# Performance work log

Hardware: AMD Instinct MI355X
Metric: run time of the kernel (lower is better)

The kernel has to match this reference:

```python
import jax, jax.numpy as jnp
import numpy as np

DIM = 1024
NUM_HEADS = 16
HEAD_DIM = DIM // NUM_HEADS
SCALE = HEAD_DIM ** (-0.5)


def setup_inputs() -> dict:
    key = jax.random.key(0)
    ks = jax.random.split(key, 10)
    b, nq, nkv = 1, 4096, 4096
    s = DIM ** -0.5
    return {
        "q": jax.random.normal(ks[0], (b, nq, DIM), jnp.float32),
        "kv": jax.random.normal(ks[1], (b, nkv, DIM), jnp.float32),
        "q_w": jax.random.normal(ks[2], (DIM, DIM), jnp.float32) * s,
        "q_b": jnp.zeros((DIM,), jnp.float32),
        "k_w": jax.random.normal(ks[3], (DIM, DIM), jnp.float32) * s,
        "k_b": jnp.zeros((DIM,), jnp.float32),
        "v_w": jax.random.normal(ks[4], (DIM, DIM), jnp.float32) * s,
        "v_b": jnp.zeros((DIM,), jnp.float32),
        "o_w": jax.random.normal(ks[5], (DIM, DIM), jnp.float32) * s,
        "o_b": jnp.zeros((DIM,), jnp.float32),
    }


def reference(q, kv, q_w, q_b, k_w, k_b, v_w, v_b, o_w, o_b):
    b, nq, _ = q.shape
    nkv = kv.shape[1]
    h, c = NUM_HEADS, HEAD_DIM
    # projections (torch Linear: x @ W^T + b); split into heads
    qh = (q @ q_w.T + q_b).reshape(b, nq, h, c).transpose(0, 2, 1, 3)   # b h nq c
    kh = (kv @ k_w.T + k_b).reshape(b, nkv, h, c).transpose(0, 2, 1, 3)  # b h nkv c
    vh = (kv @ v_w.T + v_b).reshape(b, nkv, h, c).transpose(0, 2, 1, 3)  # b h nkv c
    # full attention score matrix (non-fused, as in source)
    attn = jnp.einsum('bhqc,bhkc->bhqk', qh, kh) * SCALE
    attn = jax.nn.softmax(attn, axis=-1)
    out = jnp.einsum('bhqk,bhkc->bhqc', attn, vh)  # b h nq c
    out = out.transpose(0, 2, 1, 3).reshape(b, nq, h * c)
    out = out @ o_w.T + o_b
    return out
```

## Files before the change

### kernel.cpp

```cpp
#include <hip/hip_runtime.h>


typedef unsigned short ushort_t;
typedef unsigned short ushort4v __attribute__((ext_vector_type(4)));
typedef unsigned short ushort8 __attribute__((ext_vector_type(8)));
typedef __bf16 bf16x8 __attribute__((ext_vector_type(8)));
typedef float f32x4 __attribute__((ext_vector_type(4)));
typedef float f32x16 __attribute__((ext_vector_type(16)));

#define SEQ 4096
#define DIM 1024
#define NH 16
#define HD 64
#define QSCALE 0.18033688011112042f

#define LSTR 40
#define ABUF (128 * LSTR)
#define BBUF (64 * LSTR)

__device__ inline ushort_t fcvt(float f) {
    return __builtin_bit_cast(ushort_t, (__bf16)f);
}
__device__ inline bf16x8 frag_of(ushort8 t) {
    return __builtin_bit_cast(bf16x8, t);
}
__device__ inline bf16x8 lds_frag(const ushort_t* p) {
    return frag_of(*(const ushort8*)p);
}

__global__ __launch_bounds__(256) void cvt2(
    const float* __restrict__ s0, ushort_t* __restrict__ d0,
    const float* __restrict__ s1, ushort_t* __restrict__ d1, int n8)
{
    const float* s = blockIdx.y ? s1 : s0;
    ushort_t*    d = blockIdx.y ? d1 : d0;
    int i = blockIdx.x * 256 + threadIdx.x;
    if (i >= n8) return;
    const f32x4* sp = (const f32x4*)s + (size_t)i * 2;
    f32x4 a = sp[0], b = sp[1];
    ushort8 o;
    for (int k = 0; k < 4; ++k) { o[k] = fcvt(a[k]); o[k + 4] = fcvt(b[k]); }
    *((ushort8*)d + i) = o;
}

__global__ __launch_bounds__(256) void cvt4(
    const float* __restrict__ s0, ushort_t* __restrict__ d0,
    const float* __restrict__ s1, ushort_t* __restrict__ d1,
    const float* __restrict__ s2, ushort_t* __restrict__ d2,
    const float* __restrict__ s3, ushort_t* __restrict__ d3, int n8)
{
    const float* ss[4] = {s0, s1, s2, s3};
    ushort_t*    dd[4] = {d0, d1, d2, d3};
    const float* s = ss[blockIdx.y];
    ushort_t*    d = dd[blockIdx.y];
    int i = blockIdx.x * 256 + threadIdx.x;
    if (i >= n8) return;
    const f32x4* sp = (const f32x4*)s + (size_t)i * 2;
    f32x4 a = sp[0], b = sp[1];
    ushort8 o;
    for (int k = 0; k < 4; ++k) { o[k] = fcvt(a[k]); o[k + 4] = fcvt(b[k]); }
    *((ushort8*)d + i) = o;
}

__device__ __attribute__((always_inline)) inline void gemm_core(
    const ushort_t* __restrict__ A, const ushort_t* __restrict__ W,
    int m0, int n0, int tid, f32x4 (&acc)[4][2], ushort_t* sA, ushort_t* sB)
{
    const int lane = tid & 63;
    const int quad = lane >> 4;
    const int l15  = lane & 15;
    const int wm   = (tid >> 6) >> 1;
    const int wn   = (tid >> 6) & 1;

    const int ar0 = tid >> 2;
    const int ar1 = (tid + 256) >> 2;
    const int ac  = (tid & 3) << 3;
    const int br  = tid >> 2;
    const ushort_t* Ag0 = A + (size_t)(m0 + ar0) * DIM + ac;
    const ushort_t* Ag1 = A + (size_t)(m0 + ar1) * DIM + ac;
    const ushort_t* Wg  = W + (size_t)(n0 + br) * DIM + ac;
    const int la0 = ar0 * LSTR + ac, la1 = ar1 * LSTR + ac, lb = br * LSTR + ac;

    *(ushort8*)(sA + la0) = *(const ushort8*)(Ag0);
    *(ushort8*)(sA + la1) = *(const ushort8*)(Ag1);
    *(ushort8*)(sB + lb)  = *(const ushort8*)(Wg);
    __syncthreads();

    for (int it = 0; it < DIM / 32; ++it) {
        const int cur = it & 1;
        const int ktn = (it + 1) * 32;
        ushort_t* aC = sA + cur * ABUF;
        ushort_t* bC = sB + cur * BBUF;

        ushort8 ga0, ga1, gb0;
        if (ktn < DIM) {
            ga0 = *(const ushort8*)(Ag0 + ktn);
            ga1 = *(const ushort8*)(Ag1 + ktn);
            gb0 = *(const ushort8*)(Wg + ktn);
        }

        bf16x8 af[4], bf[2];
        for (int i = 0; i < 4; ++i)
            af[i] = lds_frag(aC + (wm * 64 + i * 16 + l15) * LSTR + quad * 8);
        for (int j = 0; j < 2; ++j)
            bf[j] = lds_frag(bC + (wn * 32 + j * 16 + l15) * LSTR + quad * 8);
        for (int i = 0; i < 4; ++i)
            for (int j = 0; j < 2; ++j)
                acc[i][j] = __builtin_amdgcn_mfma_f32_16x16x32_bf16(
                    af[i], bf[j], acc[i][j], 0, 0, 0);

        if (ktn < DIM) {
            ushort_t* aN = sA + (cur ^ 1) * ABUF;
            ushort_t* bN = sB + (cur ^ 1) * BBUF;
            *(ushort8*)(aN + la0) = ga0;
            *(ushort8*)(aN + la1) = ga1;
            *(ushort8*)(bN + lb)  = gb0;
        }
        __syncthreads();
    }
}

__global__ __launch_bounds__(256) void proj3(
    const ushort_t* __restrict__ Qb, const ushort_t* __restrict__ KVb,
    const ushort_t* __restrict__ qwb, const ushort_t* __restrict__ kwb,
    const ushort_t* __restrict__ vwb,
    const float* __restrict__ q_b, const float* __restrict__ k_b,
    const float* __restrict__ v_b,
    ushort_t* __restrict__ Qp, ushort_t* __restrict__ Kp,
    ushort_t* __restrict__ VpT)
{
    __shared__ __align__(16) ushort_t sA[2 * ABUF];
    __shared__ __align__(16) ushort_t sB[2 * BBUF];

    const int z = blockIdx.z;
    const ushort_t* A = z ? KVb : Qb;
    const ushort_t* W = (z == 0) ? qwb : (z == 1 ? kwb : vwb);
    const float* bias = (z == 0) ? q_b : (z == 1 ? k_b : v_b);
    const int tid = threadIdx.x;
    const int m0 = blockIdx.y * 128;
    const int n0 = blockIdx.x * 64;

    f32x4 acc[4][2] = {};
    gemm_core(A, W, m0, n0, tid, acc, sA, sB);

    const int lane = tid & 63, quad = lane >> 4, l15 = lane & 15;
    const int wm = (tid >> 6) >> 1, wn = (tid >> 6) & 1;
    const float scale = (z == 0) ? QSCALE : 1.0f;

    for (int j = 0; j < 2; ++j) {
        int col = n0 + wn * 32 + j * 16 + l15;
        float bj = bias[col];
        for (int i = 0; i < 4; ++i) {
            int row = m0 + wm * 64 + i * 16 + quad * 4;
            if (z == 2) {
                ushort4v o4;
                for (int r = 0; r < 4; ++r) o4[r] = fcvt(acc[i][j][r] + bj);
                *(ushort4v*)(VpT + (size_t)col * SEQ + row) = o4;
            } else {
                ushort_t* C = z ? Kp : Qp;
                for (int r = 0; r < 4; ++r)
                    C[(size_t)(row + r) * DIM + col] =
                        fcvt((acc[i][j][r] + bj) * scale);
            }
        }
    }
}

__global__ __launch_bounds__(256) void gemm_out(
    const ushort_t* __restrict__ A, const ushort_t* __restrict__ W,
    const float* __restrict__ bias, float* __restrict__ C)
{
    __shared__ __align__(16) ushort_t sA[2 * ABUF];
    __shared__ __align__(16) ushort_t sB[2 * BBUF];

    const int tid = threadIdx.x;
    const int m0 = blockIdx.y * 128;
    const int n0 = blockIdx.x * 64;

    f32x4 acc[4][2] = {};
    gemm_core(A, W, m0, n0, tid, acc, sA, sB);

    const int lane = tid & 63, quad = lane >> 4, l15 = lane & 15;
    const int wm = (tid >> 6) >> 1, wn = (tid >> 6) & 1;
    for (int j = 0; j < 2; ++j) {
        int col = n0 + wn * 32 + j * 16 + l15;
        float bj = bias[col];
        for (int i = 0; i < 4; ++i) {
            int row = m0 + wm * 64 + i * 16 + quad * 4;
            for (int r = 0; r < 4; ++r)
                C[(size_t)(row + r) * DIM + col] = acc[i][j][r] + bj;
        }
    }
}

#define BUFE (2 * 64 * 72)
__global__ __launch_bounds__(256) void attn_kernel(
    const ushort_t* __restrict__ Q, const ushort_t* __restrict__ K,
    const ushort_t* __restrict__ VT, ushort_t* __restrict__ O)
{
    __shared__ __align__(16) ushort_t sB[2 * BUFE];

    const int tid  = threadIdx.x;
    const int w    = tid >> 6;
    const int lane = tid & 63;
    const int l31  = lane & 31;
    const int hi   = lane >> 5;
    const int h    = blockIdx.x;
    const int q0   = blockIdx.y * 128 + w * 32;
    const int hHD  = h * HD;

    const int srow0 = tid >> 3;
    const int srow1 = (tid + 256) >> 3;
    const int sch   = (tid & 7) << 3;
    const ushort_t* Kg0 = K  + (size_t)srow0 * DIM + hHD + sch;
    const ushort_t* Kg1 = K  + (size_t)srow1 * DIM + hHD + sch;
    const ushort_t* Vg0 = VT + (size_t)(hHD + srow0) * SEQ + sch;
    const ushort_t* Vg1 = VT + (size_t)(hHD + srow1) * SEQ + sch;
    const int l0 = srow0 * 72 + sch, l1 = srow1 * 72 + sch;

    const ushort_t* qb = Q + (size_t)(q0 + l31) * DIM + hHD + hi * 8;
    bf16x8 qf[4];
    for (int ks = 0; ks < 4; ++ks)
        qf[ks] = frag_of(*(const ushort8*)(qb + ks * 16));

    *(ushort8*)(sB + l0)        = *(const ushort8*)(Kg0);
    *(ushort8*)(sB + l1)        = *(const ushort8*)(Kg1);
    *(ushort8*)(sB + 4608 + l0) = *(const ushort8*)(Vg0);
    *(ushort8*)(sB + 4608 + l1) = *(const ushort8*)(Vg1);
    __syncthreads();

    f32x16 oacc[2] = {};
    float l_i = 0.f;

    for (int it = 0; it < SEQ / 64; ++it) {
        const int cur = it & 1;
        const int kvn = (it + 1) * 64;
        ushort_t* bK = sB + cur * BUFE;
        ushort_t* bV = bK + 4608;

        ushort8 gk0, gk1, gv0, gv1;
        if (kvn < SEQ) {
            gk0 = *(const ushort8*)(Kg0 + (size_t)kvn * DIM);
            gk1 = *(const ushort8*)(Kg1 + (size_t)kvn * DIM);
            gv0 = *(const ushort8*)(Vg0 + kvn);
            gv1 = *(const ushort8*)(Vg1 + kvn);
        }

        bf16x8 kf[8], vf[8];
        for (int t = 0; t < 2; ++t)
            for (int ks = 0; ks < 4; ++ks)
                kf[t * 4 + ks] = lds_frag(bK + (t * 32 + l31) * 72 + ks * 16 + hi * 8);
        for (int ks = 0; ks < 4; ++ks)
            for (int dt = 0; dt < 2; ++dt)
                vf[ks * 2 + dt] = lds_frag(bV + (dt * 32 + l31) * 72 + ks * 16 + hi * 8);

        f32x16 sacc[2] = {};
        for (int t = 0; t < 2; ++t)
            for (int ks = 0; ks < 4; ++ks)
                sacc[t] = __builtin_amdgcn_mfma_f32_32x32x16_bf16(
                    kf[t * 4 + ks], qf[ks], sacc[t], 0, 0, 0);

        __syncthreads();

        float lp = 0.f;
        for (int t = 0; t < 2; ++t)
            for (int r = 0; r < 16; ++r) {
                float p = __builtin_amdgcn_exp2f(sacc[t][r]);
                sacc[t][r] = p;
                lp += p;
            }
        l_i += lp + __shfl_xor(lp, 32);

        ushort_t* pw = bK + w * 2304;
        for (int t = 0; t < 2; ++t)
            for (int g = 0; g < 4; ++g) {
                ushort4v pk;
                for (int r = 0; r < 4; ++r) pk[r] = fcvt(sacc[t][g * 4 + r]);
                *(ushort4v*)(pw + l31 * 72 + t * 32 + g * 8 + hi * 4) = pk;
            }

        for (int ks = 0; ks < 4; ++ks) {
            bf16x8 pf = lds_frag(pw + l31 * 72 + ks * 16 + hi * 8);
            for (int dt = 0; dt < 2; ++dt)
                oacc[dt] = __builtin_amdgcn_mfma_f32_32x32x16_bf16(
                    vf[ks * 2 + dt], pf, oacc[dt], 0, 0, 0);
        }

        if (kvn < SEQ) {
            ushort_t* nB = sB + (cur ^ 1) * BUFE;
            *(ushort8*)(nB + l0)        = gk0;
            *(ushort8*)(nB + l1)        = gk1;
            *(ushort8*)(nB + 4608 + l0) = gv0;
            *(ushort8*)(nB + 4608 + l1) = gv1;
        }
        __syncthreads();
    }

    float inv = 1.f / l_i;
    int qrow = q0 + l31;
    for (int dt = 0; dt < 2; ++dt)
        for (int g = 0; g < 4; ++g) {
            ushort4v o4;
            for (int r = 0; r < 4; ++r) o4[r] = fcvt(oacc[dt][g * 4 + r] * inv);
            *(ushort4v*)(O + (size_t)qrow * DIM + hHD + dt * 32 + g * 8 + hi * 4) = o4;
        }
}

extern "C" void kernel_launch(void* const* d_in, const int* in_sizes, int n_in,
                              void* d_out, int out_size, void* d_ws, size_t ws_size,
                              hipStream_t stream)
{
    const float* q   = (const float*)d_in[0];
    const float* kv  = (const float*)d_in[1];
    const float* q_w = (const float*)d_in[2];
    const float* q_b = (const float*)d_in[3];
    const float* k_w = (const float*)d_in[4];
    const float* k_b = (const float*)d_in[5];
    const float* v_w = (const float*)d_in[6];
    const float* v_b = (const float*)d_in[7];
    const float* o_w = (const float*)d_in[8];
    const float* o_b = (const float*)d_in[9];
    float* out = (float*)d_out;

    const size_t SD = (size_t)SEQ * DIM;
    const size_t WW = (size_t)DIM * DIM;
    ushort_t* Qp  = (ushort_t*)d_ws;
    ushort_t* Kp  = Qp + SD;
    ushort_t* VpT = Kp + SD;
    ushort_t* AO  = VpT + SD;
    ushort_t* Qb  = AO;
    ushort_t* KVb = AO + SD;
    ushort_t* qwb = KVb + SD;
    ushort_t* kwb = qwb + WW;
    ushort_t* vwb = kwb + WW;
    ushort_t* owb = vwb + WW;

    cvt2<<<dim3((unsigned)(SD / 8 / 256), 2), 256, 0, stream>>>(
        q, Qb, kv, KVb, (int)(SD / 8));
    cvt4<<<dim3((unsigned)(WW / 8 / 256), 4), 256, 0, stream>>>(
        q_w, qwb, k_w, kwb, v_w, vwb, o_w, owb, (int)(WW / 8));

    proj3<<<dim3(DIM / 64, SEQ / 128, 3), 256, 0, stream>>>(
        Qb, KVb, qwb, kwb, vwb, q_b, k_b, v_b, Qp, Kp, VpT);
    attn_kernel<<<dim3(NH, SEQ / 128), 256, 0, stream>>>(Qp, Kp, VpT, AO);
    gemm_out<<<dim3(DIM / 64, SEQ / 128), 256, 0, stream>>>(AO, owb, o_b, out);
}
```

Measured before the change: 273.7 us.

## Keep P in registers via permlane swap, swizzle LDS, stage V transpose

The attention kernel no longer round-trips the softmax probabilities through shared memory. It packs them to bf16 in registers and rearranges them with v_permlane32_swap into the MFMA B-operand layout, which also removes one barrier per iteration. K/V tiles switch from padded rows to an XOR-swizzled 64-wide layout that shrinks LDS use, and launch bounds now request two blocks per CU. The V projection epilogue transposes through shared memory so global writes to VpT are coalesced 16-byte stores. The risks are correctness of the register permutation layout and extra register pressure under the occupancy hint.

After: 259.3 us. 5.2% less time.

```diff
diff --git a/kernel.cpp b/kernel.cpp
--- a/kernel.cpp
+++ b/kernel.cpp
@@ -7,6 +7,7 @@
 typedef __bf16 bf16x8 __attribute__((ext_vector_type(8)));
 typedef float f32x4 __attribute__((ext_vector_type(4)));
 typedef float f32x16 __attribute__((ext_vector_type(16)));
+typedef unsigned int uint4v __attribute__((ext_vector_type(4)));
 
 #define SEQ 4096
 #define DIM 1024
@@ -26,6 +27,15 @@
 }
 __device__ inline bf16x8 lds_frag(const ushort_t* p) {
     return frag_of(*(const ushort8*)p);
+}
+__device__ inline unsigned pk2(float a, float b) {
+    return (unsigned)fcvt(a) | ((unsigned)fcvt(b) << 16);
+}
+__device__ inline void plswap(unsigned& a, unsigned& b) {
+    asm("v_permlane32_swap_b32 %0, %1" : "+v"(a), "+v"(b));
+}
+__device__ inline int swz(int row, int col) {
+    return row * 64 + (col ^ ((row & 7) << 3));
 }
 
 __global__ __launch_bounds__(256) void cvt2(
@@ -145,19 +155,34 @@
 
     const int lane = tid & 63, quad = lane >> 4, l15 = lane & 15;
     const int wm = (tid >> 6) >> 1, wn = (tid >> 6) & 1;
-    const float scale = (z == 0) ? QSCALE : 1.0f;
-
-    for (int j = 0; j < 2; ++j) {
-        int col = n0 + wn * 32 + j * 16 + l15;
-        float bj = bias[col];
-        for (int i = 0; i < 4; ++i) {
-            int row = m0 + wm * 64 + i * 16 + quad * 4;
-            if (z == 2) {
+
+    if (z == 2) {
+        const int TSTR = 136;
+        for (int j = 0; j < 2; ++j) {
+            int col = wn * 32 + j * 16 + l15;
+            float bj = bias[n0 + col];
+            for (int i = 0; i < 4; ++i) {
+                int row = wm * 64 + i * 16 + quad * 4;
                 ushort4v o4;
                 for (int r = 0; r < 4; ++r) o4[r] = fcvt(acc[i][j][r] + bj);
-                *(ushort4v*)(VpT + (size_t)col * SEQ + row) = o4;
-            } else {
-                ushort_t* C = z ? Kp : Qp;
+                *(ushort4v*)(sA + col * TSTR + row) = o4;
+            }
+        }
+        __syncthreads();
+        const int vrow = tid >> 2;
+        const int vc   = (tid & 3) << 3;
+        ushort_t* dst = VpT + (size_t)(n0 + vrow) * SEQ + m0;
+        const ushort_t* src = sA + vrow * TSTR;
+        for (int k = 0; k < 4; ++k)
+            *(ushort8*)(dst + vc + k * 32) = *(const ushort8*)(src + vc + k * 32);
+    } else {
+        const float scale = (z == 0) ? QSCALE : 1.0f;
+        ushort_t* C = z ? Kp : Qp;
+        for (int j = 0; j < 2; ++j) {
+            int col = n0 + wn * 32 + j * 16 + l15;
+            float bj = bias[col];
+            for (int i = 0; i < 4; ++i) {
+                int row = m0 + wm * 64 + i * 16 + quad * 4;
                 for (int r = 0; r < 4; ++r)
                     C[(size_t)(row + r) * DIM + col] =
                         fcvt((acc[i][j][r] + bj) * scale);
@@ -193,8 +218,9 @@
     }
 }
 
-#define BUFE (2 * 64 * 72)
-__global__ __launch_bounds__(256) void attn_kernel(
+#define TILE 4096
+#define BUFE (2 * TILE)
+__global__ __launch_bounds__(256, 2) void attn_kernel(
     const ushort_t* __restrict__ Q, const ushort_t* __restrict__ K,
     const ushort_t* __restrict__ VT, ushort_t* __restrict__ O)
 {
@@ -210,23 +236,23 @@
     const int hHD  = h * HD;
 
     const int srow0 = tid >> 3;
-    const int srow1 = (tid + 256) >> 3;
+    const int srow1 = srow0 + 32;
     const int sch   = (tid & 7) << 3;
     const ushort_t* Kg0 = K  + (size_t)srow0 * DIM + hHD + sch;
     const ushort_t* Kg1 = K  + (size_t)srow1 * DIM + hHD + sch;
     const ushort_t* Vg0 = VT + (size_t)(hHD + srow0) * SEQ + sch;
     const ushort_t* Vg1 = VT + (size_t)(hHD + srow1) * SEQ + sch;
-    const int l0 = srow0 * 72 + sch, l1 = srow1 * 72 + sch;
+    const int lk0 = swz(srow0, sch), lk1 = swz(srow1, sch);
 
     const ushort_t* qb = Q + (size_t)(q0 + l31) * DIM + hHD + hi * 8;
     bf16x8 qf[4];
     for (int ks = 0; ks < 4; ++ks)
         qf[ks] = frag_of(*(const ushort8*)(qb + ks * 16));
 
-    *(ushort8*)(sB + l0)        = *(const ushort8*)(Kg0);
-    *(ushort8*)(sB + l1)        = *(const ushort8*)(Kg1);
-    *(ushort8*)(sB + 4608 + l0) = *(const ushort8*)(Vg0);
-    *(ushort8*)(sB + 4608 + l1) = *(const ushort8*)(Vg1);
+    *(ushort8*)(sB + lk0)        = *(const ushort8*)(Kg0);
+    *(ushort8*)(sB + lk1)        = *(const ushort8*)(Kg1);
+    *(ushort8*)(sB + TILE + lk0) = *(const ushort8*)(Vg0);
+    *(ushort8*)(sB + TILE + lk1) = *(const ushort8*)(Vg1);
     __syncthreads();
 
     f32x16 oacc[2] = {};
@@ -236,7 +262,7 @@
         const int cur = it & 1;
         const int kvn = (it + 1) * 64;
         ushort_t* bK = sB + cur * BUFE;
-        ushort_t* bV = bK + 4608;
+        ushort_t* bV = bK + TILE;
 
         ushort8 gk0, gk1, gv0, gv1;
         if (kvn < SEQ) {
@@ -248,19 +274,21 @@
 
         bf16x8 kf[8], vf[8];
         for (int t = 0; t < 2; ++t)
-            for (int ks = 0; ks < 4; ++ks)
-                kf[t * 4 + ks] = lds_frag(bK + (t * 32 + l31) * 72 + ks * 16 + hi * 8);
-        for (int ks = 0; ks < 4; ++ks)
-            for (int dt = 0; dt < 2; ++dt)
-                vf[ks * 2 + dt] = lds_frag(bV + (dt * 32 + l31) * 72 + ks * 16 + hi * 8);
+            for (int ks = 0; ks < 4; ++ks) {
+                int r = t * 32 + l31;
+                kf[t * 4 + ks] = lds_frag(bK + swz(r, ks * 16 + hi * 8));
+            }
+        for (int dt = 0; dt < 2; ++dt)
+            for (int ks = 0; ks < 4; ++ks) {
+                int r = dt * 32 + l31;
+                vf[ks * 2 + dt] = lds_frag(bV + swz(r, ks * 16 + hi * 8));
+            }
 
         f32x16 sacc[2] = {};
         for (int t = 0; t < 2; ++t)
             for (int ks = 0; ks < 4; ++ks)
                 sacc[t] = __builtin_amdgcn_mfma_f32_32x32x16_bf16(
                     kf[t * 4 + ks], qf[ks], sacc[t], 0, 0, 0);
-
-        __syncthreads();
 
         float lp = 0.f;
         for (int t = 0; t < 2; ++t)
@@ -271,16 +299,16 @@
             }
         l_i += lp + __shfl_xor(lp, 32);
 
-        ushort_t* pw = bK + w * 2304;
-        for (int t = 0; t < 2; ++t)
-            for (int g = 0; g < 4; ++g) {
-                ushort4v pk;
-                for (int r = 0; r < 4; ++r) pk[r] = fcvt(sacc[t][g * 4 + r]);
-                *(ushort4v*)(pw + l31 * 72 + t * 32 + g * 8 + hi * 4) = pk;
-            }
-
         for (int ks = 0; ks < 4; ++ks) {
-            bf16x8 pf = lds_frag(pw + l31 * 72 + ks * 16 + hi * 8);
+            const int t = ks >> 1, s8 = (ks & 1) * 8;
+            unsigned p00 = pk2(sacc[t][s8 + 0], sacc[t][s8 + 1]);
+            unsigned p01 = pk2(sacc[t][s8 + 2], sacc[t][s8 + 3]);
+            unsigned p10 = pk2(sacc[t][s8 + 4], sacc[t][s8 + 5]);
+            unsigned p11 = pk2(sacc[t][s8 + 6], sacc[t][s8 + 7]);
+            plswap(p00, p10);
+            plswap(p01, p11);
+            uint4v wv; wv[0] = p00; wv[1] = p01; wv[2] = p10; wv[3] = p11;
+            bf16x8 pf = __builtin_bit_cast(bf16x8, wv);
             for (int dt = 0; dt < 2; ++dt)
                 oacc[dt] = __builtin_amdgcn_mfma_f32_32x32x16_bf16(
                     vf[ks * 2 + dt], pf, oacc[dt], 0, 0, 0);
@@ -288,10 +316,10 @@
 
         if (kvn < SEQ) {
             ushort_t* nB = sB + (cur ^ 1) * BUFE;
-            *(ushort8*)(nB + l0)        = gk0;
-            *(ushort8*)(nB + l1)        = gk1;
-            *(ushort8*)(nB + 4608 + l0) = gv0;
-            *(ushort8*)(nB + 4608 + l1) = gv1;
+            *(ushort8*)(nB + lk0)        = gk0;
+            *(ushort8*)(nB + lk1)        = gk1;
+            *(ushort8*)(nB + TILE + lk0) = gv0;
+            *(ushort8*)(nB + TILE + lk1) = gv1;
         }
         __syncthreads();
     }
```
